# Optimization experiments

Measured on AMD Instinct MI355X. Metric: run time of the kernel, lower is better.

Reference implementation:

```python
import jax, jax.numpy as jnp
import numpy as np

B, I, H, O = 256, 4096, 4096, 4096

def setup_inputs() -> dict:
    key = jax.random.key(0)
    ks = jax.random.split(key, 8)
    s_ih = 1.0 / np.sqrt(H)
    return {
        "x": jax.random.normal(ks[0], (B, I), jnp.float32),
        "h0": jax.random.normal(ks[1], (1, B, H), jnp.float32),
        "w_ih": jax.random.uniform(ks[2], (H, I), jnp.float32, -s_ih, s_ih),
        "b_ih": jax.random.uniform(ks[3], (H,), jnp.float32, -s_ih, s_ih),
        "w_hh": jax.random.uniform(ks[4], (H, H), jnp.float32, -s_ih, s_ih),
        "b_hh": jax.random.uniform(ks[5], (H,), jnp.float32, -s_ih, s_ih),
        "w_lin": jax.random.uniform(ks[6], (O, H), jnp.float32, -s_ih, s_ih),
        "b_lin": jax.random.uniform(ks[7], (O,), jnp.float32, -s_ih, s_ih),
    }

def reference(x, h0, w_ih, b_ih, w_hh, b_hh, w_lin, b_lin):
    # Single-step Elman RNN cell (seq_len=1, num_layers=1):
    # h' = tanh(x @ W_ih^T + b_ih + h @ W_hh^T + b_hh)
    h = h0[0]                                   # [B, H]
    hn = jnp.tanh(x @ w_ih.T + b_ih + h @ w_hh.T + b_hh)  # [B, H]
    logits = hn @ w_lin.T + b_lin               # [B, O]
    probs = jax.nn.softmax(logits, axis=-1)
    # rr has leading seq dim of 1; hn keeps [num_layers, B, H]
    return probs[None, :, :], hn[None, :, :]
```

## Files before the change

kernel.cpp:

```cpp
#include <hip/hip_runtime.h>
#include <hip/hip_bf16.h>
#include <cstdint>


using short8 = __attribute__((ext_vector_type(8))) short;
using f32x4  = __attribute__((ext_vector_type(4))) float;

#define HDIM 4096

__device__ __forceinline__ short bfbits(float f) {
    __bf16 b = (__bf16)f;
    return __builtin_bit_cast(short, b);
}
__device__ __forceinline__ short8 pack8(const float4& a, const float4& b) {
    short8 r;
    r[0] = bfbits(a.x); r[1] = bfbits(a.y); r[2] = bfbits(a.z); r[3] = bfbits(a.w);
    r[4] = bfbits(b.x); r[5] = bfbits(b.y); r[6] = bfbits(b.z); r[7] = bfbits(b.w);
    return r;
}

template<int MODE>
__global__ __launch_bounds__(512) void rnn_gemm(
    const float* __restrict__ A0, const float* __restrict__ W0,
    const float* __restrict__ A1, const float* __restrict__ W1,
    float* __restrict__ out, int steps, int kslice)
{
    __shared__ __align__(16) unsigned char smem[65536];

    const int t    = threadIdx.x;
    const int lane = t & 63;
    const int wid  = t >> 6;
    const int bid  = blockIdx.x;
    const int grp   = bid & 7;
    const int ntile = bid >> 3;
    const int mtile = grp >> 2;
    const int ks    = grp & 3;
    const int m0 = mtile * 128, n0 = ntile * 128;
    const int wr = (wid & 3) * 32;
    const int wc = (wid >> 2) * 64;
    const int lr = lane & 15;
    const int lk = lane >> 4;

    const float* As; const float* Ws; int koff;
    if (MODE == 0) {
        if (ks < 2) { As = A0; Ws = W0; koff = ks * kslice; }
        else        { As = A1; Ws = W1; koff = (ks - 2) * kslice; }
    } else { As = A0; Ws = W0; koff = ks * kslice; }

    const int lr8 = lane >> 3;
    const int ch  = lane & 7;
    const int rbase = wid * 16;

    float4 pa0, pa1, pa2, pa3, pb0, pb1, pb2, pb3;
    float4 qa0, qa1, qa2, qa3, qb0, qb1, qb2, qb3;

#define ISSUE(A0r, A1r, A2r, A3r, B0r, B1r, B2r, B3r, step)                     \
    {                                                                           \
        const int kb = koff + (step) * 64 + ch * 8;                             \
        const float* ap = As + (size_t)(m0 + rbase + lr8) * HDIM + kb;          \
        const float* wp = Ws + (size_t)(n0 + rbase + lr8) * HDIM + kb;          \
        A0r = *(const float4*)(ap);            A1r = *(const float4*)(ap + 4);  \
        A2r = *(const float4*)(ap + 8 * HDIM); A3r = *(const float4*)(ap + 8 * HDIM + 4); \
        B0r = *(const float4*)(wp);            B1r = *(const float4*)(wp + 4);  \
        B2r = *(const float4*)(wp + 8 * HDIM); B3r = *(const float4*)(wp + 8 * HDIM + 4); \
    }

#define WRITEBUF(A0r, A1r, A2r, A3r, B0r, B1r, B2r, B3r, b)                     \
    {                                                                           \
        unsigned char* base = smem + (b) * 32768;                               \
        const int r0 = rbase + lr8, r1 = rbase + 8 + lr8;                       \
        const int o0 = r0 * 128 + ((ch ^ (r0 & 7)) * 16);                       \
        const int o1 = r1 * 128 + ((ch ^ (r1 & 7)) * 16);                       \
        *(short8*)(base + o0)         = pack8(A0r, A1r);                        \
        *(short8*)(base + o1)         = pack8(A2r, A3r);                        \
        *(short8*)(base + 16384 + o0) = pack8(B0r, B1r);                        \
        *(short8*)(base + 16384 + o1) = pack8(B2r, B3r);                        \
    }

    f32x4 acc[2][4];
#pragma unroll
    for (int i = 0; i < 2; ++i)
#pragma unroll
        for (int j = 0; j < 4; ++j) acc[i][j] = (f32x4){0.f, 0.f, 0.f, 0.f};

    auto compute = [&](int b) {
        const unsigned char* base = smem + b * 32768;
#pragma unroll
        for (int s = 0; s < 2; ++s) {
            short8 af[2], bv[4];
#pragma unroll
            for (int mr = 0; mr < 2; ++mr) {
                const int r = wr + mr * 16 + lr;
                af[mr] = *(const short8*)(base + r * 128 + (((s * 4 + lk) ^ (r & 7)) * 16));
            }
#pragma unroll
            for (int nr = 0; nr < 4; ++nr) {
                const int r = wc + nr * 16 + lr;
                bv[nr] = *(const short8*)(base + 16384 + r * 128 + (((s * 4 + lk) ^ (r & 7)) * 16));
            }
#pragma unroll
            for (int mr = 0; mr < 2; ++mr)
#pragma unroll
                for (int nr = 0; nr < 4; ++nr)
                    acc[mr][nr] = __builtin_amdgcn_mfma_f32_16x16x32_bf16(
                        af[mr], bv[nr], acc[mr][nr], 0, 0, 0);
        }
    };

    ISSUE(pa0, pa1, pa2, pa3, pb0, pb1, pb2, pb3, 0);
    ISSUE(qa0, qa1, qa2, qa3, qb0, qb1, qb2, qb3, 1);
    asm volatile("s_waitcnt vmcnt(8)" ::: "memory");
    WRITEBUF(pa0, pa1, pa2, pa3, pb0, pb1, pb2, pb3, 0);
    asm volatile("s_waitcnt lgkmcnt(0)" ::: "memory");
    __builtin_amdgcn_s_barrier();

    for (int tt = 0; tt < steps; tt += 2) {
        if (tt + 2 < steps) ISSUE(pa0, pa1, pa2, pa3, pb0, pb1, pb2, pb3, tt + 2);
        compute(0);
        if (tt + 2 < steps) { asm volatile("s_waitcnt vmcnt(8)" ::: "memory"); }
        else                { asm volatile("s_waitcnt vmcnt(0)" ::: "memory"); }
        WRITEBUF(qa0, qa1, qa2, qa3, qb0, qb1, qb2, qb3, 1);
        asm volatile("s_waitcnt lgkmcnt(0)" ::: "memory");
        __builtin_amdgcn_s_barrier();

        if (tt + 3 < steps) ISSUE(qa0, qa1, qa2, qa3, qb0, qb1, qb2, qb3, tt + 3);
        compute(1);
        if (tt + 2 < steps) {
            if (tt + 3 < steps) { asm volatile("s_waitcnt vmcnt(8)" ::: "memory"); }
            else                { asm volatile("s_waitcnt vmcnt(0)" ::: "memory"); }
            WRITEBUF(pa0, pa1, pa2, pa3, pb0, pb1, pb2, pb3, 0);
            asm volatile("s_waitcnt lgkmcnt(0)" ::: "memory");
        }
        __builtin_amdgcn_s_barrier();
    }
#undef ISSUE
#undef WRITEBUF

#pragma unroll
    for (int mr = 0; mr < 2; ++mr)
#pragma unroll
        for (int nr = 0; nr < 4; ++nr) {
            const int n = n0 + wc + nr * 16 + lr;
#pragma unroll
            for (int e = 0; e < 4; ++e) {
                const int m = m0 + wr + mr * 16 + lk * 4 + e;
                atomicAdd(&out[(size_t)m * HDIM + n], acc[mr][nr][e]);
            }
        }
}

__global__ __launch_bounds__(256) void finish_hn(
    float* __restrict__ hn, const float* __restrict__ b_ih,
    const float* __restrict__ b_hh)
{
    const int idx = blockIdx.x * 256 + threadIdx.x;
    const int col = (idx & 1023) * 4;
    f32x4 v  = *((const f32x4*)hn + idx);
    f32x4 bi = *(const f32x4*)(b_ih + col);
    f32x4 bh = *(const f32x4*)(b_hh + col);
#pragma unroll
    for (int j = 0; j < 4; ++j) v[j] = tanhf(v[j] + bi[j] + bh[j]);
    *((f32x4*)hn + idx) = v;
}

__global__ __launch_bounds__(256) void softmax_bias(
    float* __restrict__ p, const float* __restrict__ bl)
{
    const int row = blockIdx.x;
    float* rp = p + (size_t)row * HDIM;
    const int t = threadIdx.x;

    f32x4 v[4];
#pragma unroll
    for (int i = 0; i < 4; ++i) {
        const int c = t + i * 256;
        v[i] = *(const f32x4*)(rp + c * 4);
        f32x4 b = *(const f32x4*)(bl + c * 4);
        v[i] += b;
    }

    float mx = -1e30f;
#pragma unroll
    for (int i = 0; i < 4; ++i)
#pragma unroll
        for (int j = 0; j < 4; ++j) mx = fmaxf(mx, v[i][j]);
#pragma unroll
    for (int off = 32; off; off >>= 1) mx = fmaxf(mx, __shfl_xor(mx, off));

    __shared__ float red[4];
    if ((t & 63) == 0) red[t >> 6] = mx;
    __syncthreads();
    mx = fmaxf(fmaxf(red[0], red[1]), fmaxf(red[2], red[3]));

    float sum = 0.f;
#pragma unroll
    for (int i = 0; i < 4; ++i)
#pragma unroll
        for (int j = 0; j < 4; ++j) {
            float e = __expf(v[i][j] - mx);
            v[i][j] = e;
            sum += e;
        }
#pragma unroll
    for (int off = 32; off; off >>= 1) sum += __shfl_xor(sum, off);

    __syncthreads();
    if ((t & 63) == 0) red[t >> 6] = sum;
    __syncthreads();
    sum = (red[0] + red[1]) + (red[2] + red[3]);

    const float inv = 1.f / sum;
#pragma unroll
    for (int i = 0; i < 4; ++i) {
        f32x4 o = v[i];
#pragma unroll
        for (int j = 0; j < 4; ++j) o[j] *= inv;
        *(f32x4*)(rp + (t + i * 256) * 4) = o;
    }
}

extern "C" void kernel_launch(void* const* d_in, const int* in_sizes, int n_in,
                              void* d_out, int out_size, void* d_ws, size_t ws_size,
                              hipStream_t stream) {
    const float* x     = (const float*)d_in[0];
    const float* h0    = (const float*)d_in[1];
    const float* w_ih  = (const float*)d_in[2];
    const float* b_ih  = (const float*)d_in[3];
    const float* w_hh  = (const float*)d_in[4];
    const float* b_hh  = (const float*)d_in[5];
    const float* w_lin = (const float*)d_in[6];
    const float* b_lin = (const float*)d_in[7];

    float* probs = (float*)d_out;
    float* hn    = (float*)d_out + 256 * HDIM;

    hipMemsetAsync(d_out, 0, (size_t)2 * 256 * HDIM * sizeof(float), stream);

    rnn_gemm<0><<<256, 512, 0, stream>>>(x, w_ih, h0, w_hh, hn, 32, 2048);
    finish_hn<<<1024, 256, 0, stream>>>(hn, b_ih, b_hh);
    rnn_gemm<1><<<256, 512, 0, stream>>>(hn, w_lin, nullptr, nullptr, probs, 16, 1024);
    softmax_bias<<<256, 256, 0, stream>>>(probs, b_lin);
}
```

Measured before the change: 261.9 us.

## Enlarge GEMM tiles to 256x256 with 1024 threads and 16-way split-K

```diff
diff --git a/kernel.cpp b/kernel.cpp
--- a/kernel.cpp
+++ b/kernel.cpp
@@ -20,86 +20,83 @@
 }
 
 template<int MODE>
-__global__ __launch_bounds__(512) void rnn_gemm(
+__global__ __launch_bounds__(1024) void rnn_gemm(
     const float* __restrict__ A0, const float* __restrict__ W0,
     const float* __restrict__ A1, const float* __restrict__ W1,
     float* __restrict__ out, int steps, int kslice)
 {
-    __shared__ __align__(16) unsigned char smem[65536];
+    __shared__ __align__(16) unsigned char smem[131072];
 
     const int t    = threadIdx.x;
     const int lane = t & 63;
     const int wid  = t >> 6;
     const int bid  = blockIdx.x;
-    const int grp   = bid & 7;
-    const int ntile = bid >> 3;
-    const int mtile = grp >> 2;
-    const int ks    = grp & 3;
-    const int m0 = mtile * 128, n0 = ntile * 128;
-    const int wr = (wid & 3) * 32;
-    const int wc = (wid >> 2) * 64;
+    const int ks    = bid & 15;
+    const int ntile = bid >> 4;
+    const int n0 = ntile * 256;
+    const int wrow = (wid >> 2) * 64;
+    const int wcol = (wid & 3) * 64;
     const int lr = lane & 15;
     const int lk = lane >> 4;
 
     const float* As; const float* Ws; int koff;
     if (MODE == 0) {
-        if (ks < 2) { As = A0; Ws = W0; koff = ks * kslice; }
-        else        { As = A1; Ws = W1; koff = (ks - 2) * kslice; }
+        if (ks < 8) { As = A0; Ws = W0; koff = ks * kslice; }
+        else        { As = A1; Ws = W1; koff = (ks - 8) * kslice; }
     } else { As = A0; Ws = W0; koff = ks * kslice; }
 
-    const int lr8 = lane >> 3;
-    const int ch  = lane & 7;
+    const int lr8   = lane >> 3;
+    const int ch    = lane & 7;
     const int rbase = wid * 16;
 
-    float4 pa0, pa1, pa2, pa3, pb0, pb1, pb2, pb3;
-    float4 qa0, qa1, qa2, qa3, qb0, qb1, qb2, qb3;
-
-#define ISSUE(A0r, A1r, A2r, A3r, B0r, B1r, B2r, B3r, step)                     \
+    float4 sa0, sa1, sa2, sa3, sb0, sb1, sb2, sb3;
+
+#define ISSUE(step)                                                             \
     {                                                                           \
         const int kb = koff + (step) * 64 + ch * 8;                             \
-        const float* ap = As + (size_t)(m0 + rbase + lr8) * HDIM + kb;          \
+        const float* ap = As + (size_t)(rbase + lr8) * HDIM + kb;               \
         const float* wp = Ws + (size_t)(n0 + rbase + lr8) * HDIM + kb;          \
-        A0r = *(const float4*)(ap);            A1r = *(const float4*)(ap + 4);  \
-        A2r = *(const float4*)(ap + 8 * HDIM); A3r = *(const float4*)(ap + 8 * HDIM + 4); \
-        B0r = *(const float4*)(wp);            B1r = *(const float4*)(wp + 4);  \
-        B2r = *(const float4*)(wp + 8 * HDIM); B3r = *(const float4*)(wp + 8 * HDIM + 4); \
-    }
-
-#define WRITEBUF(A0r, A1r, A2r, A3r, B0r, B1r, B2r, B3r, b)                     \
+        sa0 = *(const float4*)(ap);            sa1 = *(const float4*)(ap + 4);  \
+        sa2 = *(const float4*)(ap + 8 * HDIM); sa3 = *(const float4*)(ap + 8 * HDIM + 4); \
+        sb0 = *(const float4*)(wp);            sb1 = *(const float4*)(wp + 4);  \
+        sb2 = *(const float4*)(wp + 8 * HDIM); sb3 = *(const float4*)(wp + 8 * HDIM + 4); \
+    }
+
+#define WRITEBUF(b)                                                             \
     {                                                                           \
-        unsigned char* base = smem + (b) * 32768;                               \
-        const int r0 = rbase + lr8, r1 = rbase + 8 + lr8;                       \
+        unsigned char* base = smem + (b) * 65536;                               \
+        const int r0 = rbase + lr8, r1 = r0 + 8;                                \
         const int o0 = r0 * 128 + ((ch ^ (r0 & 7)) * 16);                       \
         const int o1 = r1 * 128 + ((ch ^ (r1 & 7)) * 16);                       \
-        *(short8*)(base + o0)         = pack8(A0r, A1r);                        \
-        *(short8*)(base + o1)         = pack8(A2r, A3r);                        \
-        *(short8*)(base + 16384 + o0) = pack8(B0r, B1r);                        \
-        *(short8*)(base + 16384 + o1) = pack8(B2r, B3r);                        \
-    }
-
-    f32x4 acc[2][4];
-#pragma unroll
-    for (int i = 0; i < 2; ++i)
+        *(short8*)(base + o0)         = pack8(sa0, sa1);                        \
+        *(short8*)(base + o1)         = pack8(sa2, sa3);                        \
+        *(short8*)(base + 32768 + o0) = pack8(sb0, sb1);                        \
+        *(short8*)(base + 32768 + o1) = pack8(sb2, sb3);                        \
+    }
+
+    f32x4 acc[4][4];
+#pragma unroll
+    for (int i = 0; i < 4; ++i)
 #pragma unroll
         for (int j = 0; j < 4; ++j) acc[i][j] = (f32x4){0.f, 0.f, 0.f, 0.f};
 
     auto compute = [&](int b) {
-        const unsigned char* base = smem + b * 32768;
+        const unsigned char* base = smem + b * 65536;
 #pragma unroll
         for (int s = 0; s < 2; ++s) {
-            short8 af[2], bv[4];
-#pragma unroll
-            for (int mr = 0; mr < 2; ++mr) {
-                const int r = wr + mr * 16 + lr;
+            short8 af[4], bv[4];
+#pragma unroll
+            for (int mr = 0; mr < 4; ++mr) {
+                const int r = wrow + mr * 16 + lr;
                 af[mr] = *(const short8*)(base + r * 128 + (((s * 4 + lk) ^ (r & 7)) * 16));
             }
 #pragma unroll
             for (int nr = 0; nr < 4; ++nr) {
-                const int r = wc + nr * 16 + lr;
-                bv[nr] = *(const short8*)(base + 16384 + r * 128 + (((s * 4 + lk) ^ (r & 7)) * 16));
+                const int r = wcol + nr * 16 + lr;
+                bv[nr] = *(const short8*)(base + 32768 + r * 128 + (((s * 4 + lk) ^ (r & 7)) * 16));
             }
 #pragma unroll
-            for (int mr = 0; mr < 2; ++mr)
+            for (int mr = 0; mr < 4; ++mr)
 #pragma unroll
                 for (int nr = 0; nr < 4; ++nr)
                     acc[mr][nr] = __builtin_amdgcn_mfma_f32_16x16x32_bf16(
@@ -107,28 +104,19 @@
         }
     };
 
-    ISSUE(pa0, pa1, pa2, pa3, pb0, pb1, pb2, pb3, 0);
-    ISSUE(qa0, qa1, qa2, qa3, qb0, qb1, qb2, qb3, 1);
-    asm volatile("s_waitcnt vmcnt(8)" ::: "memory");
-    WRITEBUF(pa0, pa1, pa2, pa3, pb0, pb1, pb2, pb3, 0);
+    ISSUE(0);
+    asm volatile("s_waitcnt vmcnt(0)" ::: "memory");
+    WRITEBUF(0);
+    ISSUE(1);
     asm volatile("s_waitcnt lgkmcnt(0)" ::: "memory");
     __builtin_amdgcn_s_barrier();
 
-    for (int tt = 0; tt < steps; tt += 2) {
-        if (tt + 2 < steps) ISSUE(pa0, pa1, pa2, pa3, pb0, pb1, pb2, pb3, tt + 2);
-        compute(0);
-        if (tt + 2 < steps) { asm volatile("s_waitcnt vmcnt(8)" ::: "memory"); }
-        else                { asm volatile("s_waitcnt vmcnt(0)" ::: "memory"); }
-        WRITEBUF(qa0, qa1, qa2, qa3, qb0, qb1, qb2, qb3, 1);
-        asm volatile("s_waitcnt lgkmcnt(0)" ::: "memory");
-        __builtin_amdgcn_s_barrier();
-
-        if (tt + 3 < steps) ISSUE(qa0, qa1, qa2, qa3, qb0, qb1, qb2, qb3, tt + 3);
-        compute(1);
-        if (tt + 2 < steps) {
-            if (tt + 3 < steps) { asm volatile("s_waitcnt vmcnt(8)" ::: "memory"); }
-            else                { asm volatile("s_waitcnt vmcnt(0)" ::: "memory"); }
-            WRITEBUF(pa0, pa1, pa2, pa3, pb0, pb1, pb2, pb3, 0);
+    for (int tt = 0; tt < steps; ++tt) {
+        compute(tt & 1);
+        if (tt + 1 < steps) {
+            asm volatile("s_waitcnt vmcnt(0)" ::: "memory");
+            WRITEBUF((tt + 1) & 1);
+            if (tt + 2 < steps) ISSUE(tt + 2);
             asm volatile("s_waitcnt lgkmcnt(0)" ::: "memory");
         }
         __builtin_amdgcn_s_barrier();
@@ -137,13 +125,13 @@
 #undef WRITEBUF
 
 #pragma unroll
-    for (int mr = 0; mr < 2; ++mr)
+    for (int mr = 0; mr < 4; ++mr)
 #pragma unroll
         for (int nr = 0; nr < 4; ++nr) {
-            const int n = n0 + wc + nr * 16 + lr;
+            const int n = n0 + wcol + nr * 16 + lr;
 #pragma unroll
             for (int e = 0; e < 4; ++e) {
-                const int m = m0 + wr + mr * 16 + lk * 4 + e;
+                const int m = wrow + mr * 16 + lk * 4 + e;
                 atomicAdd(&out[(size_t)m * HDIM + n], acc[mr][nr][e]);
             }
         }
@@ -236,8 +224,10 @@
 
     hipMemsetAsync(d_out, 0, (size_t)2 * 256 * HDIM * sizeof(float), stream);
 
-    rnn_gemm<0><<<256, 512, 0, stream>>>(x, w_ih, h0, w_hh, hn, 32, 2048);
+    rnn_gemm<0><<<256, 1024, 0, stream>>>(x, w_ih, h0, w_hh, hn,
+                                          8, 512);
     finish_hn<<<1024, 256, 0, stream>>>(hn, b_ih, b_hh);
-    rnn_gemm<1><<<256, 512, 0, stream>>>(hn, w_lin, nullptr, nullptr, probs, 16, 1024);
+    rnn_gemm<1><<<256, 1024, 0, stream>>>(hn, w_lin, nullptr, nullptr, probs,
+                                          4, 256);
     softmax_bias<<<256, 256, 0, stream>>>(probs, b_lin);
 }
```

Result: slower. 332.5 us (+27.0%).
